# Optimization experiments

Hardware: AMD Instinct MI355X
Metric: run time of the kernel (lower is better)

The kernel has to match this reference:

```python
import jax, jax.numpy as jnp
import numpy as np

N_FFT = 1024
HOP_LENGTH = 256
N_BANDS = 128


def setup_inputs() -> dict:
    key = jax.random.key(0)
    k1, k2 = jax.random.split(key)
    B, C, T = 16, 1, 1001
    filter_bands = jax.random.uniform(k1, (B, C, N_BANDS, T), dtype=jnp.float32)
    # uniform [0,1); reference applies *2-1 to match torch.rand(...)*2-1
    noise = jax.random.uniform(k2, (B, C, (T - 1) * HOP_LENGTH), dtype=jnp.float32)
    return {"filter_bands": filter_bands, "noise": noise}


def reference(filter_bands, noise):
    B, C, F_bands, T = filter_bands.shape
    pad = N_FFT // 2

    noise = noise * 2.0 - 1.0                      # [-1, 1)
    padded = jnp.pad(noise, ((0, 0), (0, 0), (pad, pad)))  # (B,C,L+N_FFT)

    # unfold: T frames of length N_FFT with stride HOP_LENGTH
    frame_idx = np.arange(T)[:, None] * HOP_LENGTH + np.arange(N_FFT)[None, :]
    frames = padded[:, :, frame_idx]               # (B,C,T,N_FFT)

    # nearest-neighbor interpolation of bands to N_FFT//2 (torch 'nearest': floor(i*in/out))
    band_idx = (np.arange(N_FFT // 2) * F_bands) // (N_FFT // 2)
    filt = jnp.transpose(filter_bands, (0, 1, 3, 2))[:, :, :, band_idx]  # (B,C,T,N_FFT//2)
    dc = jnp.zeros(filt.shape[:-1] + (1,), filt.dtype)
    filt = jnp.concatenate([dc, filt], axis=-1)    # (B,C,T,N_FFT//2+1)

    spec = jnp.fft.rfft(frames)                    # complex64 (B,C,T,513)
    y = jnp.fft.irfft(filt * spec, n=N_FFT)        # (B,C,T,N_FFT)

    # hann window, periodic=False: 0.5*(1 - cos(2*pi*n/(N-1)))
    n = jnp.arange(N_FFT, dtype=y.dtype)
    win = 0.5 * (1.0 - jnp.cos(2.0 * jnp.pi * n / (N_FFT - 1)))
    y = y * win

    # fold = overlap-add
    Lp = padded.shape[-1]
    out = jnp.zeros((B, C, Lp), y.dtype).at[:, :, frame_idx].add(y)
    return out[:, :, pad:-pad]
```

## Files before the change

### kernel.cpp

```cpp
#include <hip/hip_runtime.h>
#include <math.h>

#define NFFT   1024
#define HOP    256
#define NBANDS 128
#define TFRM   1001
#define BB     16
#define NLEN   256000
#define PADL   512
#define NPAIRS 501

#define PX(a) ((a) + ((a) >> 4))

__global__ __launch_bounds__(256) void zero_and_tables(
    float4* __restrict__ out4, int n4, float* __restrict__ ws)
{
    const int tid = blockIdx.x * 256 + threadIdx.x;
    const float4 z = make_float4(0.0f, 0.0f, 0.0f, 0.0f);
    for (int i = tid; i < n4; i += gridDim.x * 256) out4[i] = z;
    if (tid < 256) {
        float s_, c_;
        sincosf(-6.283185307179586f * (float)tid * (1.0f / 1024.0f), &s_, &c_);
        ws[2 * tid]     = c_;
        ws[2 * tid + 1] = s_;
    } else if (tid < 1280) {
        const int k = tid - 256;
        ws[512 + k] = 0.5f * (1.0f - cosf(6.283185307179586f * (float)k * (1.0f / 1023.0f)))
                      * (1.0f / 1024.0f);
    }
}

template<int NS, int SGN>
__device__ __forceinline__ void r4stage2(const float2* __restrict__ x,
                                         float2* __restrict__ y,
                                         const float2* __restrict__ tw, int j) {
    const int m = j & (NS - 1);
    const float2 a0 = x[PX(j)];
    const float2 a1 = x[PX(j + 256)];
    const float2 a2 = x[PX(j + 512)];
    const float2 a3 = x[PX(j + 768)];
    float v1r, v1i, v2r, v2i, v3r, v3i;
    {
        const float2 w = tw[m * (256 / NS)];
        const float wr1 = w.x, wi1 = (SGN < 0) ? w.y : -w.y;
        const float wr2 = wr1 * wr1 - wi1 * wi1, wi2 = 2.0f * wr1 * wi1;
        const float wr3 = wr2 * wr1 - wi2 * wi1, wi3 = wr2 * wi1 + wi2 * wr1;
        v1r = a1.x * wr1 - a1.y * wi1; v1i = a1.x * wi1 + a1.y * wr1;
        v2r = a2.x * wr2 - a2.y * wi2; v2i = a2.x * wi2 + a2.y * wr2;
        v3r = a3.x * wr3 - a3.y * wi3; v3i = a3.x * wi3 + a3.y * wr3;
    }
    const float t0r = a0.x + v2r, t0i = a0.y + v2i;
    const float t1r = a0.x - v2r, t1i = a0.y - v2i;
    const float t2r = v1r + v3r,  t2i = v1i + v3i;
    const float ur  = v1r - v3r,  ui  = v1i - v3i;
    const float t3r = (SGN < 0) ? ui  : -ui;
    const float t3i = (SGN < 0) ? -ur : ur;
    const int d = ((j & ~(NS - 1)) << 2) + m;
    y[PX(d)]          = make_float2(t0r + t2r, t0i + t2i);
    y[PX(d + NS)]     = make_float2(t1r + t3r, t1i + t3i);
    y[PX(d + 2*NS)]   = make_float2(t0r - t2r, t0i - t2i);
    y[PX(d + 3*NS)]   = make_float2(t1r - t3r, t1i - t3i);
}

__global__ __launch_bounds__(256) void fn_kernel(
    const float* __restrict__ fb,
    const float* __restrict__ noise,
    const float* __restrict__ tbl,
    float* __restrict__ out)
{
    __shared__ float2 b0[1087], b1[1087];
    __shared__ float2 tw[256];
    __shared__ float2 gab[128];

    const int tid = threadIdx.x;
    const int hw  = blockIdx.x;
    const int blk = (hw & 7) * 1002 + (hw >> 3);
    const int b   = blk / NPAIRS;
    const int p   = blk - b * NPAIRS;
    const int ta  = 2 * p;
    const bool has_b    = (ta + 1) < TFRM;
    const bool interior = (p >= 1) & (p <= 498);

    tw[tid] = ((const float2*)tbl)[tid & 255];
    if (tid < NBANDS) {
        const size_t off = (size_t)b * (NBANDS * TFRM) + (size_t)tid * TFRM + ta;
        const float ga_ = fb[off];
        const float gb_ = has_b ? fb[off + 1] : 0.0f;
        gab[tid] = make_float2(ga_, gb_);
    }

    const float* nb = noise + (size_t)b * NLEN;
    const int base = ta * HOP - PADL;
    float2 a0, a1, a2, a3;
    if (interior) {
        const int g = base + tid;
        const float v0 = __builtin_fmaf(nb[g],        2.0f, -1.0f);
        const float v1 = __builtin_fmaf(nb[g + 256],  2.0f, -1.0f);
        const float v2 = __builtin_fmaf(nb[g + 512],  2.0f, -1.0f);
        const float v3 = __builtin_fmaf(nb[g + 768],  2.0f, -1.0f);
        const float v4 = __builtin_fmaf(nb[g + 1024], 2.0f, -1.0f);
        a0 = make_float2(v0, v1);
        a1 = make_float2(v1, v2);
        a2 = make_float2(v2, v3);
        a3 = make_float2(v3, v4);
    } else {
        const int g = base + tid;
        #define LD2(gg) make_float2( \
            ((gg) >= 0 && (gg) < NLEN) ? nb[(gg)] * 2.0f - 1.0f : 0.0f, \
            (has_b && (gg) + HOP >= 0 && (gg) + HOP < NLEN) ? nb[(gg) + HOP] * 2.0f - 1.0f : 0.0f)
        a0 = LD2(g); a1 = LD2(g + 256); a2 = LD2(g + 512); a3 = LD2(g + 768);
        #undef LD2
    }
    {
        const float t0r = a0.x + a2.x, t0i = a0.y + a2.y;
        const float t1r = a0.x - a2.x, t1i = a0.y - a2.y;
        const float t2r = a1.x + a3.x, t2i = a1.y + a3.y;
        const float ur  = a1.x - a3.x, ui  = a1.y - a3.y;
        const float t3r = ui, t3i = -ur;
        const int d = 4 * tid;
        b0[PX(d)]     = make_float2(t0r + t2r, t0i + t2i);
        b0[PX(d + 1)] = make_float2(t1r + t3r, t1i + t3i);
        b0[PX(d + 2)] = make_float2(t0r - t2r, t0i - t2i);
        b0[PX(d + 3)] = make_float2(t1r - t3r, t1i - t3i);
    }
    __syncthreads();

    r4stage2<4,   -1>(b0, b1, tw, tid); __syncthreads();
    r4stage2<16,  -1>(b1, b0, tw, tid); __syncthreads();
    r4stage2<64,  -1>(b0, b1, tw, tid); __syncthreads();
    r4stage2<256, -1>(b1, b0, tw, tid); __syncthreads();

    {
        float2 W[4];
        #pragma unroll
        for (int c = 0; c < 4; ++c) {
            const int k = tid + 256 * c;
            const float2 z1 = b0[PX(k)];
            const float2 z2 = b0[PX((NFFT - k) & (NFFT - 1))];
            if (k == 0) {
                W[c] = make_float2(0.0f, 0.0f);
            } else {
                const int jm = (k < NFFT - k) ? k : NFFT - k;
                const float2 g = gab[(jm - 1) >> 2];
                const float Far = 0.5f * (z1.x + z2.x), Fai = 0.5f * (z1.y - z2.y);
                const float Fbr = 0.5f * (z1.y + z2.y), Fbi = 0.5f * (z2.x - z1.x);
                W[c] = make_float2(g.x * Far - g.y * Fbi, g.x * Fai + g.y * Fbr);
            }
        }
        const float t0r = W[0].x + W[2].x, t0i = W[0].y + W[2].y;
        const float t1r = W[0].x - W[2].x, t1i = W[0].y - W[2].y;
        const float t2r = W[1].x + W[3].x, t2i = W[1].y + W[3].y;
        const float ur  = W[1].x - W[3].x, ui  = W[1].y - W[3].y;
        const float t3r = -ui, t3i = ur;
        const int d = 4 * tid;
        b1[PX(d)]     = make_float2(t0r + t2r, t0i + t2i);
        b1[PX(d + 1)] = make_float2(t1r + t3r, t1i + t3i);
        b1[PX(d + 2)] = make_float2(t0r - t2r, t0i - t2i);
        b1[PX(d + 3)] = make_float2(t1r - t3r, t1i - t3i);
    }
    __syncthreads();

    r4stage2<4,  +1>(b1, b0, tw, tid); __syncthreads();
    r4stage2<16, +1>(b0, b1, tw, tid); __syncthreads();
    r4stage2<64, +1>(b1, b0, tw, tid); __syncthreads();

    {
        const float2 c0 = b0[PX(tid)];
        const float2 c1 = b0[PX(tid + 256)];
        const float2 c2 = b0[PX(tid + 512)];
        const float2 c3 = b0[PX(tid + 768)];
        const float2 w = tw[tid];
        const float wr1 = w.x, wi1 = -w.y;
        const float wr2 = wr1 * wr1 - wi1 * wi1, wi2 = 2.0f * wr1 * wi1;
        const float wr3 = wr2 * wr1 - wi2 * wi1, wi3 = wr2 * wi1 + wi2 * wr1;
        const float v1r = c1.x * wr1 - c1.y * wi1, v1i = c1.x * wi1 + c1.y * wr1;
        const float v2r = c2.x * wr2 - c2.y * wi2, v2i = c2.x * wi2 + c2.y * wr2;
        const float v3r = c3.x * wr3 - c3.y * wi3, v3i = c3.x * wi3 + c3.y * wr3;
        const float t0r = c0.x + v2r, t0i = c0.y + v2i;
        const float t1r = c0.x - v2r, t1i = c0.y - v2i;
        const float t2r = v1r + v3r,  t2i = v1i + v3i;
        const float ur  = v1r - v3r,  ui  = v1i - v3i;
        const float t3r = -ui, t3i = ur;
        float2 r[4];
        r[0] = make_float2(t0r + t2r, t0i + t2i);
        r[1] = make_float2(t1r + t3r, t1i + t3i);
        r[2] = make_float2(t0r - t2r, t0i - t2i);
        r[3] = make_float2(t1r - t3r, t1i - t3i);

        const float* win = tbl + 512;
        float wv[4];
        #pragma unroll
        for (int c = 0; c < 4; ++c) wv[c] = win[tid + 256 * c];
        float s[5];
        s[0] = r[0].x * wv[0];
        s[1] = r[1].x * wv[1] + r[0].y * wv[0];
        s[2] = r[2].x * wv[2] + r[1].y * wv[1];
        s[3] = r[3].x * wv[3] + r[2].y * wv[2];
        s[4] =                  r[3].y * wv[3];

        float* ob = out + (size_t)b * NLEN;
        if (interior) {
            #pragma unroll
            for (int c = 0; c < 5; ++c) {
                atomicAdd(&ob[base + tid + 256 * c], s[c]);
            }
        } else {
            #pragma unroll
            for (int c = 0; c < 5; ++c) {
                const int pa = base + tid + 256 * c;
                if (pa >= 0 && pa < NLEN) atomicAdd(&ob[pa], s[c]);
            }
        }
    }
}

extern "C" void kernel_launch(void* const* d_in, const int* in_sizes, int n_in,
                              void* d_out, int out_size, void* d_ws, size_t ws_size,
                              hipStream_t stream) {
    const float* fb    = (const float*)d_in[0];
    const float* noise = (const float*)d_in[1];
    float* out = (float*)d_out;
    float* tbl = (float*)d_ws;

    zero_and_tables<<<2048, 256, 0, stream>>>((float4*)out, out_size / 4, tbl);

    const int grid = BB * NPAIRS;
    fn_kernel<<<grid, 256, 0, stream>>>(fb, noise, tbl, out);
}
```

Baseline: 110.1 us.

## Process four frames per block and overlap-add locally to cut atomics

Each block now handles two complex FFT pairs (four consecutive frames) instead of one. The window-weighted outputs of those frames are summed in registers, so one of the seven output segments per block is fully covered locally and written with a plain store instead of an atomic. This reduces global atomic traffic and per-block setup such as loading the twiddle table. In exchange shared memory doubles, which may lower occupancy, and the grid halves.

```diff
diff --git a/kernel.cpp b/kernel.cpp
--- a/kernel.cpp
+++ b/kernel.cpp
@@ -8,7 +8,7 @@
 #define BB     16
 #define NLEN   256000
 #define PADL   512
-#define NPAIRS 501
+#define QPB    251
 
 #define PX(a) ((a) + ((a) >> 4))
 
@@ -62,38 +62,13 @@
     y[PX(d + 3*NS)]   = make_float2(t1r - t3r, t1i - t3i);
 }
 
-__global__ __launch_bounds__(256) void fn_kernel(
-    const float* __restrict__ fb,
-    const float* __restrict__ noise,
-    const float* __restrict__ tbl,
-    float* __restrict__ out)
-{
-    __shared__ float2 b0[1087], b1[1087];
-    __shared__ float2 tw[256];
-    __shared__ float2 gab[128];
-
-    const int tid = threadIdx.x;
-    const int hw  = blockIdx.x;
-    const int blk = (hw & 7) * 1002 + (hw >> 3);
-    const int b   = blk / NPAIRS;
-    const int p   = blk - b * NPAIRS;
-    const int ta  = 2 * p;
-    const bool has_b    = (ta + 1) < TFRM;
-    const bool interior = (p >= 1) & (p <= 498);
-
-    tw[tid] = ((const float2*)tbl)[tid & 255];
-    if (tid < NBANDS) {
-        const size_t off = (size_t)b * (NBANDS * TFRM) + (size_t)tid * TFRM + ta;
-        const float ga_ = fb[off];
-        const float gb_ = has_b ? fb[off + 1] : 0.0f;
-        gab[tid] = make_float2(ga_, gb_);
-    }
-
-    const float* nb = noise + (size_t)b * NLEN;
-    const int base = ta * HOP - PADL;
+__device__ __forceinline__ void load_stage0(
+    const float* __restrict__ nb, int base, int tid,
+    bool fast, bool has_b, float2* __restrict__ dst)
+{
     float2 a0, a1, a2, a3;
-    if (interior) {
-        const int g = base + tid;
+    const int g = base + tid;
+    if (fast) {
         const float v0 = __builtin_fmaf(nb[g],        2.0f, -1.0f);
         const float v1 = __builtin_fmaf(nb[g + 256],  2.0f, -1.0f);
         const float v2 = __builtin_fmaf(nb[g + 512],  2.0f, -1.0f);
@@ -104,111 +79,164 @@
         a2 = make_float2(v2, v3);
         a3 = make_float2(v3, v4);
     } else {
-        const int g = base + tid;
         #define LD2(gg) make_float2( \
             ((gg) >= 0 && (gg) < NLEN) ? nb[(gg)] * 2.0f - 1.0f : 0.0f, \
             (has_b && (gg) + HOP >= 0 && (gg) + HOP < NLEN) ? nb[(gg) + HOP] * 2.0f - 1.0f : 0.0f)
         a0 = LD2(g); a1 = LD2(g + 256); a2 = LD2(g + 512); a3 = LD2(g + 768);
         #undef LD2
     }
-    {
-        const float t0r = a0.x + a2.x, t0i = a0.y + a2.y;
-        const float t1r = a0.x - a2.x, t1i = a0.y - a2.y;
-        const float t2r = a1.x + a3.x, t2i = a1.y + a3.y;
-        const float ur  = a1.x - a3.x, ui  = a1.y - a3.y;
-        const float t3r = ui, t3i = -ur;
-        const int d = 4 * tid;
-        b0[PX(d)]     = make_float2(t0r + t2r, t0i + t2i);
-        b0[PX(d + 1)] = make_float2(t1r + t3r, t1i + t3i);
-        b0[PX(d + 2)] = make_float2(t0r - t2r, t0i - t2i);
-        b0[PX(d + 3)] = make_float2(t1r - t3r, t1i - t3i);
-    }
+    const float t0r = a0.x + a2.x, t0i = a0.y + a2.y;
+    const float t1r = a0.x - a2.x, t1i = a0.y - a2.y;
+    const float t2r = a1.x + a3.x, t2i = a1.y + a3.y;
+    const float ur  = a1.x - a3.x, ui  = a1.y - a3.y;
+    const float t3r = ui, t3i = -ur;
+    const int d = 4 * tid;
+    dst[PX(d)]     = make_float2(t0r + t2r, t0i + t2i);
+    dst[PX(d + 1)] = make_float2(t1r + t3r, t1i + t3i);
+    dst[PX(d + 2)] = make_float2(t0r - t2r, t0i - t2i);
+    dst[PX(d + 3)] = make_float2(t1r - t3r, t1i - t3i);
+}
+
+__device__ __forceinline__ void herm_inv0(
+    const float2* __restrict__ src, float2* __restrict__ dst,
+    const float2* __restrict__ gab, int tid)
+{
+    float2 W[4];
+    #pragma unroll
+    for (int c = 0; c < 4; ++c) {
+        const int k = tid + 256 * c;
+        const float2 z1 = src[PX(k)];
+        const float2 z2 = src[PX((NFFT - k) & (NFFT - 1))];
+        if (k == 0) {
+            W[c] = make_float2(0.0f, 0.0f);
+        } else {
+            const int jm = (k < NFFT - k) ? k : NFFT - k;
+            const float2 g = gab[(jm - 1) >> 2];
+            const float Far = 0.5f * (z1.x + z2.x), Fai = 0.5f * (z1.y - z2.y);
+            const float Fbr = 0.5f * (z1.y + z2.y), Fbi = 0.5f * (z2.x - z1.x);
+            W[c] = make_float2(g.x * Far - g.y * Fbi, g.x * Fai + g.y * Fbr);
+        }
+    }
+    const float t0r = W[0].x + W[2].x, t0i = W[0].y + W[2].y;
+    const float t1r = W[0].x - W[2].x, t1i = W[0].y - W[2].y;
+    const float t2r = W[1].x + W[3].x, t2i = W[1].y + W[3].y;
+    const float ur  = W[1].x - W[3].x, ui  = W[1].y - W[3].y;
+    const float t3r = -ui, t3i = ur;
+    const int d = 4 * tid;
+    dst[PX(d)]     = make_float2(t0r + t2r, t0i + t2i);
+    dst[PX(d + 1)] = make_float2(t1r + t3r, t1i + t3i);
+    dst[PX(d + 2)] = make_float2(t0r - t2r, t0i - t2i);
+    dst[PX(d + 3)] = make_float2(t1r - t3r, t1i - t3i);
+}
+
+__device__ __forceinline__ void inv_final(
+    const float2* __restrict__ src, const float2* __restrict__ tw, int tid,
+    float2 r[4])
+{
+    const float2 c0 = src[PX(tid)];
+    const float2 c1 = src[PX(tid + 256)];
+    const float2 c2 = src[PX(tid + 512)];
+    const float2 c3 = src[PX(tid + 768)];
+    const float2 w = tw[tid];
+    const float wr1 = w.x, wi1 = -w.y;
+    const float wr2 = wr1 * wr1 - wi1 * wi1, wi2 = 2.0f * wr1 * wi1;
+    const float wr3 = wr2 * wr1 - wi2 * wi1, wi3 = wr2 * wi1 + wi2 * wr1;
+    const float v1r = c1.x * wr1 - c1.y * wi1, v1i = c1.x * wi1 + c1.y * wr1;
+    const float v2r = c2.x * wr2 - c2.y * wi2, v2i = c2.x * wi2 + c2.y * wr2;
+    const float v3r = c3.x * wr3 - c3.y * wi3, v3i = c3.x * wi3 + c3.y * wr3;
+    const float t0r = c0.x + v2r, t0i = c0.y + v2i;
+    const float t1r = c0.x - v2r, t1i = c0.y - v2i;
+    const float t2r = v1r + v3r,  t2i = v1i + v3i;
+    const float ur  = v1r - v3r,  ui  = v1i - v3i;
+    const float t3r = -ui, t3i = ur;
+    r[0] = make_float2(t0r + t2r, t0i + t2i);
+    r[1] = make_float2(t1r + t3r, t1i + t3i);
+    r[2] = make_float2(t0r - t2r, t0i - t2i);
+    r[3] = make_float2(t1r - t3r, t1i - t3i);
+}
+
+__global__ __launch_bounds__(256) void fn_kernel(
+    const float* __restrict__ fb,
+    const float* __restrict__ noise,
+    const float* __restrict__ tbl,
+    float* __restrict__ out)
+{
+    __shared__ float2 bA0[1087], bA1[1087], bB0[1087], bB1[1087];
+    __shared__ float2 tw[256];
+    __shared__ float2 gabA[128], gabB[128];
+
+    const int tid = threadIdx.x;
+    const int hw  = blockIdx.x;
+    const int blk = (hw & 7) * 502 + (hw >> 3);
+    const int b   = blk / QPB;
+    const int q   = blk - b * QPB;
+    const bool interior = (q >= 1) & (q <= 248);
+    const int  f0 = 4 * q;
+    const bool has_bA = (f0 + 1) < TFRM;
+    const bool validB = (f0 + 2) < TFRM;
+    const bool has_bB = (f0 + 3) < TFRM;
+
+    tw[tid] = ((const float2*)tbl)[tid & 255];
+    if (tid < NBANDS) {
+        const size_t off = (size_t)b * (NBANDS * TFRM) + (size_t)tid * TFRM + f0;
+        gabA[tid] = make_float2(fb[off], has_bA ? fb[off + 1] : 0.0f);
+        gabB[tid] = make_float2(validB ? fb[off + 2] : 0.0f,
+                                has_bB ? fb[off + 3] : 0.0f);
+    }
+
+    const float* nb = noise + (size_t)b * NLEN;
+    const int base_a = 1024 * q - PADL;
+
+    load_stage0(nb, base_a,       tid, interior, has_bA, bA0);
+    load_stage0(nb, base_a + 512, tid, interior, has_bB, bB0);
     __syncthreads();
 
-    r4stage2<4,   -1>(b0, b1, tw, tid); __syncthreads();
-    r4stage2<16,  -1>(b1, b0, tw, tid); __syncthreads();
-    r4stage2<64,  -1>(b0, b1, tw, tid); __syncthreads();
-    r4stage2<256, -1>(b1, b0, tw, tid); __syncthreads();
-
-    {
-        float2 W[4];
+    r4stage2<4,   -1>(bA0, bA1, tw, tid); r4stage2<4,   -1>(bB0, bB1, tw, tid); __syncthreads();
+    r4stage2<16,  -1>(bA1, bA0, tw, tid); r4stage2<16,  -1>(bB1, bB0, tw, tid); __syncthreads();
+    r4stage2<64,  -1>(bA0, bA1, tw, tid); r4stage2<64,  -1>(bB0, bB1, tw, tid); __syncthreads();
+    r4stage2<256, -1>(bA1, bA0, tw, tid); r4stage2<256, -1>(bB1, bB0, tw, tid); __syncthreads();
+
+    herm_inv0(bA0, bA1, gabA, tid); herm_inv0(bB0, bB1, gabB, tid); __syncthreads();
+
+    r4stage2<4,  +1>(bA1, bA0, tw, tid); r4stage2<4,  +1>(bB1, bB0, tw, tid); __syncthreads();
+    r4stage2<16, +1>(bA0, bA1, tw, tid); r4stage2<16, +1>(bB0, bB1, tw, tid); __syncthreads();
+    r4stage2<64, +1>(bA1, bA0, tw, tid); r4stage2<64, +1>(bB1, bB0, tw, tid); __syncthreads();
+
+    float2 rA[4], rB[4];
+    inv_final(bA0, tw, tid, rA);
+    inv_final(bB0, tw, tid, rB);
+
+    const float* win = tbl + 512;
+    float wv[4];
+    #pragma unroll
+    for (int c = 0; c < 4; ++c) wv[c] = win[tid + 256 * c];
+
+    float s[7];
+    #pragma unroll
+    for (int i = 0; i < 7; ++i) s[i] = 0.0f;
+    #pragma unroll
+    for (int c = 0; c < 4; ++c) {
+        s[c]     += rA[c].x * wv[c];
+        s[c + 1] += rA[c].y * wv[c];
+        s[c + 2] += rB[c].x * wv[c];
+        s[c + 3] += rB[c].y * wv[c];
+    }
+
+    float* ob = out + (size_t)b * NLEN;
+    if (interior) {
         #pragma unroll
-        for (int c = 0; c < 4; ++c) {
-            const int k = tid + 256 * c;
-            const float2 z1 = b0[PX(k)];
-            const float2 z2 = b0[PX((NFFT - k) & (NFFT - 1))];
-            if (k == 0) {
-                W[c] = make_float2(0.0f, 0.0f);
-            } else {
-                const int jm = (k < NFFT - k) ? k : NFFT - k;
-                const float2 g = gab[(jm - 1) >> 2];
-                const float Far = 0.5f * (z1.x + z2.x), Fai = 0.5f * (z1.y - z2.y);
-                const float Fbr = 0.5f * (z1.y + z2.y), Fbi = 0.5f * (z2.x - z1.x);
-                W[c] = make_float2(g.x * Far - g.y * Fbi, g.x * Fai + g.y * Fbr);
-            }
+        for (int c = 0; c < 7; ++c) {
+            const int pos = base_a + tid + 256 * c;
+            if (c == 3) ob[pos] = s[3];
+            else atomicAdd(&ob[pos], s[c]);
         }
-        const float t0r = W[0].x + W[2].x, t0i = W[0].y + W[2].y;
-        const float t1r = W[0].x - W[2].x, t1i = W[0].y - W[2].y;
-        const float t2r = W[1].x + W[3].x, t2i = W[1].y + W[3].y;
-        const float ur  = W[1].x - W[3].x, ui  = W[1].y - W[3].y;
-        const float t3r = -ui, t3i = ur;
-        const int d = 4 * tid;
-        b1[PX(d)]     = make_float2(t0r + t2r, t0i + t2i);
-        b1[PX(d + 1)] = make_float2(t1r + t3r, t1i + t3i);
-        b1[PX(d + 2)] = make_float2(t0r - t2r, t0i - t2i);
-        b1[PX(d + 3)] = make_float2(t1r - t3r, t1i - t3i);
-    }
-    __syncthreads();
-
-    r4stage2<4,  +1>(b1, b0, tw, tid); __syncthreads();
-    r4stage2<16, +1>(b0, b1, tw, tid); __syncthreads();
-    r4stage2<64, +1>(b1, b0, tw, tid); __syncthreads();
-
-    {
-        const float2 c0 = b0[PX(tid)];
-        const float2 c1 = b0[PX(tid + 256)];
-        const float2 c2 = b0[PX(tid + 512)];
-        const float2 c3 = b0[PX(tid + 768)];
-        const float2 w = tw[tid];
-        const float wr1 = w.x, wi1 = -w.y;
-        const float wr2 = wr1 * wr1 - wi1 * wi1, wi2 = 2.0f * wr1 * wi1;
-        const float wr3 = wr2 * wr1 - wi2 * wi1, wi3 = wr2 * wi1 + wi2 * wr1;
-        const float v1r = c1.x * wr1 - c1.y * wi1, v1i = c1.x * wi1 + c1.y * wr1;
-        const float v2r = c2.x * wr2 - c2.y * wi2, v2i = c2.x * wi2 + c2.y * wr2;
-        const float v3r = c3.x * wr3 - c3.y * wi3, v3i = c3.x * wi3 + c3.y * wr3;
-        const float t0r = c0.x + v2r, t0i = c0.y + v2i;
-        const float t1r = c0.x - v2r, t1i = c0.y - v2i;
-        const float t2r = v1r + v3r,  t2i = v1i + v3i;
-        const float ur  = v1r - v3r,  ui  = v1i - v3i;
-        const float t3r = -ui, t3i = ur;
-        float2 r[4];
-        r[0] = make_float2(t0r + t2r, t0i + t2i);
-        r[1] = make_float2(t1r + t3r, t1i + t3i);
-        r[2] = make_float2(t0r - t2r, t0i - t2i);
-        r[3] = make_float2(t1r - t3r, t1i - t3i);
-
-        const float* win = tbl + 512;
-        float wv[4];
+    } else {
         #pragma unroll
-        for (int c = 0; c < 4; ++c) wv[c] = win[tid + 256 * c];
-        float s[5];
-        s[0] = r[0].x * wv[0];
-        s[1] = r[1].x * wv[1] + r[0].y * wv[0];
-        s[2] = r[2].x * wv[2] + r[1].y * wv[1];
-        s[3] = r[3].x * wv[3] + r[2].y * wv[2];
-        s[4] =                  r[3].y * wv[3];
-
-        float* ob = out + (size_t)b * NLEN;
-        if (interior) {
-            #pragma unroll
-            for (int c = 0; c < 5; ++c) {
-                atomicAdd(&ob[base + tid + 256 * c], s[c]);
-            }
-        } else {
-            #pragma unroll
-            for (int c = 0; c < 5; ++c) {
-                const int pa = base + tid + 256 * c;
-                if (pa >= 0 && pa < NLEN) atomicAdd(&ob[pa], s[c]);
+        for (int c = 0; c < 7; ++c) {
+            const int pos = base_a + tid + 256 * c;
+            if (pos >= 0 && pos < NLEN) {
+                if (c == 3) ob[pos] = s[3];
+                else atomicAdd(&ob[pos], s[c]);
             }
         }
     }
@@ -224,6 +252,6 @@
 
     zero_and_tables<<<2048, 256, 0, stream>>>((float4*)out, out_size / 4, tbl);
 
-    const int grid = BB * NPAIRS;
+    const int grid = BB * QPB;
     fn_kernel<<<grid, 256, 0, stream>>>(fb, noise, tbl, out);
 }
```

New measurement: 114.4 us. +3.9%, slower.
